# Kernel optimization log

Measured on AMD Instinct MI355X. Metric: run time of the kernel, lower is better.

The kernel has to match this reference:

```python
import jax, jax.numpy as jnp
import numpy as np

E = 1_000_000
C = 32
OUT = 64


def setup_inputs() -> dict:
    key = jax.random.key(0)
    k_x, k_nb, k_w, k_b = jax.random.split(key, 4)
    x = jax.random.normal(k_x, (E, C), dtype=jnp.float32)
    neighbors = jax.random.randint(k_nb, (E, 4), 0, E, dtype=jnp.int64)
    # Linear(5*C, OUT): weight [OUT, 5C], bias [OUT] (torch layout)
    bound = 1.0 / np.sqrt(5 * C)
    W = jax.random.uniform(k_w, (OUT, 5 * C), minval=-bound, maxval=bound, dtype=jnp.float32)
    b = jax.random.uniform(k_b, (OUT,), minval=-bound, maxval=bound, dtype=jnp.float32)
    return {"x": x, "neighbors": neighbors, "W": W, "b": b}


def reference(x, neighbors, W, b):
    # pad with a zero row so index -1 (clamped to 0 then masked) yields zeros
    padded = jnp.concatenate([x, jnp.zeros((1, x.shape[1]), dtype=x.dtype)], axis=0)
    safe = jnp.clip(neighbors, 0, None)
    nb = padded[safe]                                  # [E, 4, C]
    nb = jnp.where((neighbors < 0)[..., None], 0.0, nb)
    a0, a1, b0, b1 = nb[:, 0], nb[:, 1], nb[:, 2], nb[:, 3]
    desc_a = jnp.concatenate([a0 + a1, jnp.abs(a0 - a1)], axis=1)   # [E, 2C]
    desc_b = jnp.concatenate([b0 + b1, jnp.abs(b0 - b1)], axis=1)   # [E, 2C]
    combined = jnp.concatenate([x, desc_a + desc_b, jnp.abs(desc_a - desc_b)], axis=1)  # [E, 5C]
    return combined @ W.T + b
```

## Files before the change

kernel.cpp:

```cpp
#include <hip/hip_runtime.h>


typedef __bf16 bf16_t;
typedef __bf16 bf16x8 __attribute__((ext_vector_type(8)));
typedef float  f32x4  __attribute__((ext_vector_type(4)));

#define EC      1000000
#define CCH     32
#define OUTD    64
#define KD      160
#define MT      64
#define NTILES  (EC / MT)
#define NFRAG   1280

__global__ __launch_bounds__(256)
void meshconv_kernel(const float* __restrict__ x,
                     const int*   __restrict__ nbr,
                     const float* __restrict__ W,
                     const float* __restrict__ bias,
                     float*       __restrict__ out)
{
    __shared__ bf16_t w_lds[NFRAG * 8];

    const int tid  = threadIdx.x;
    const int wave = tid >> 6;
    const int lane = tid & 63;
    const int col  = lane & 15;
    const int quad = lane >> 4;

    for (int i = tid; i < NFRAG; i += 256) {
        const int fc  = i & 15;
        const int fq  = (i >> 4) & 3;
        const int ftn = (i >> 6) & 3;
        const int fks = i >> 8;
        const float* src = W + (ftn * 16 + fc) * KD + fks * 32 + fq * 8;
        f32x4 w0 = *(const f32x4*)src;
        f32x4 w1 = *(const f32x4*)(src + 4);
        bf16x8 wf;
        wf[0]=(bf16_t)w0[0]; wf[1]=(bf16_t)w0[1]; wf[2]=(bf16_t)w0[2]; wf[3]=(bf16_t)w0[3];
        wf[4]=(bf16_t)w1[0]; wf[5]=(bf16_t)w1[1]; wf[6]=(bf16_t)w1[2]; wf[7]=(bf16_t)w1[3];
        *(bf16x8*)&w_lds[i * 8] = wf;
    }

    float bv[4];
#pragma unroll
    for (int tn = 0; tn < 4; ++tn) bv[tn] = bias[tn * 16 + col];

    __syncthreads();

    for (int tile = blockIdx.x; tile < NTILES; tile += (int)gridDim.x) {
        const int e = tile * MT + wave * 16 + col;

        const int4 nb = ((const int4*)nbr)[e];
        const float m0 = nb.x < 0 ? 0.f : 1.f;
        const float m1 = nb.y < 0 ? 0.f : 1.f;
        const float m2 = nb.z < 0 ? 0.f : 1.f;
        const float m3 = nb.w < 0 ? 0.f : 1.f;
        const int i0 = nb.x < 0 ? 0 : nb.x;
        const int i1 = nb.y < 0 ? 0 : nb.y;
        const int i2 = nb.z < 0 ? 0 : nb.z;
        const int i3 = nb.w < 0 ? 0 : nb.w;

        const int co = quad * 8;
        const f32x4* px  = (const f32x4*)(x + (size_t)e  * CCH + co);
        const f32x4* pa0 = (const f32x4*)(x + (size_t)i0 * CCH + co);
        const f32x4* pa1 = (const f32x4*)(x + (size_t)i1 * CCH + co);
        const f32x4* pb0 = (const f32x4*)(x + (size_t)i2 * CCH + co);
        const f32x4* pb1 = (const f32x4*)(x + (size_t)i3 * CCH + co);

        f32x4 xv[2], a0[2], a1[2], b0[2], b1[2];
#pragma unroll
        for (int h = 0; h < 2; ++h) {
            xv[h] = px[h];
            a0[h] = pa0[h] * m0;
            a1[h] = pa1[h] * m1;
            b0[h] = pb0[h] * m2;
            b1[h] = pb1[h] * m3;
        }

        bf16x8 af[5];
#pragma unroll
        for (int h = 0; h < 2; ++h) {
#pragma unroll
            for (int j = 0; j < 4; ++j) {
                const int jj = h * 4 + j;
                const float sa = a0[h][j] + a1[h][j];
                const float da = fabsf(a0[h][j] - a1[h][j]);
                const float sb = b0[h][j] + b1[h][j];
                const float db = fabsf(b0[h][j] - b1[h][j]);
                af[0][jj] = (bf16_t)xv[h][j];
                af[1][jj] = (bf16_t)(sa + sb);
                af[2][jj] = (bf16_t)(da + db);
                af[3][jj] = (bf16_t)fabsf(sa - sb);
                af[4][jj] = (bf16_t)fabsf(da - db);
            }
        }

        f32x4 acc[4] = {{0.f,0.f,0.f,0.f},{0.f,0.f,0.f,0.f},
                        {0.f,0.f,0.f,0.f},{0.f,0.f,0.f,0.f}};
#pragma unroll
        for (int ks = 0; ks < 5; ++ks) {
#pragma unroll
            for (int tn = 0; tn < 4; ++tn) {
                const bf16x8 bfr = *(const bf16x8*)&w_lds[(((ks*4+tn)*4+quad)*16 + col) * 8];
                acc[tn] = __builtin_amdgcn_mfma_f32_16x16x32_bf16(af[ks], bfr, acc[tn], 0, 0, 0);
            }
        }

#pragma unroll
        for (int tn = 0; tn < 4; ++tn) {
            float* op = out + (size_t)(tile * MT + wave * 16 + quad * 4) * OUTD + tn * 16 + col;
#pragma unroll
            for (int r = 0; r < 4; ++r)
                __builtin_nontemporal_store(acc[tn][r] + bv[tn], op + (size_t)r * OUTD);
        }
    }
}

extern "C" void kernel_launch(void* const* d_in, const int* in_sizes, int n_in,
                              void* d_out, int out_size, void* d_ws, size_t ws_size,
                              hipStream_t stream) {
    const float* x    = (const float*)d_in[0];
    const int*   nbr  = (const int*)d_in[1];
    const float* W    = (const float*)d_in[2];
    const float* bias = (const float*)d_in[3];
    float* out = (float*)d_out;
    meshconv_kernel<<<dim3(3072), dim3(256), 0, stream>>>(x, nbr, W, bias, out);
}
```

Before: 436.6 us.

## Software-pipeline gathers across tiles and stage output through LDS for vector stores

Prefetches the next tile's neighbor indices and gathered rows into registers while the current tile is computed, so memory latency overlaps with the MFMA work. The accumulator results are transposed through a padded per-wave LDS buffer, which lets each lane write 16-byte contiguous nontemporal stores instead of scalar strided stores. The grid shrinks from 3072 to 1024 blocks so each block loops over more tiles. This raises register pressure from the doubled prefetch buffers, adds LDS traffic, and may reduce occupancy.

```diff
diff --git a/kernel.cpp b/kernel.cpp
--- a/kernel.cpp
+++ b/kernel.cpp
@@ -12,6 +12,8 @@
 #define MT      64
 #define NTILES  (EC / MT)
 #define NFRAG   1280
+#define TSTR    68
+#define GRID    1024
 
 __global__ __launch_bounds__(256)
 void meshconv_kernel(const float* __restrict__ x,
@@ -21,6 +23,7 @@
                      float*       __restrict__ out)
 {
     __shared__ bf16_t w_lds[NFRAG * 8];
+    __shared__ __attribute__((aligned(16))) float t_lds[4 * 16 * TSTR];
 
     const int tid  = threadIdx.x;
     const int wave = tid >> 6;
@@ -46,37 +49,41 @@
 #pragma unroll
     for (int tn = 0; tn < 4; ++tn) bv[tn] = bias[tn * 16 + col];
 
+    float* tw = &t_lds[wave * 16 * TSTR];
+
     __syncthreads();
 
-    for (int tile = blockIdx.x; tile < NTILES; tile += (int)gridDim.x) {
-        const int e = tile * MT + wave * 16 + col;
-
-        const int4 nb = ((const int4*)nbr)[e];
-        const float m0 = nb.x < 0 ? 0.f : 1.f;
-        const float m1 = nb.y < 0 ? 0.f : 1.f;
-        const float m2 = nb.z < 0 ? 0.f : 1.f;
-        const float m3 = nb.w < 0 ? 0.f : 1.f;
+    auto load_tile = [&](int t, int4& nb, f32x4* buf) {
+        const int e = t * MT + wave * 16 + col;
+        nb = ((const int4*)nbr)[e];
         const int i0 = nb.x < 0 ? 0 : nb.x;
         const int i1 = nb.y < 0 ? 0 : nb.y;
         const int i2 = nb.z < 0 ? 0 : nb.z;
         const int i3 = nb.w < 0 ? 0 : nb.w;
+        const int co = quad * 8;
+        const f32x4* p;
+        p = (const f32x4*)(x + (size_t)e  * CCH + co); buf[0] = p[0]; buf[1] = p[1];
+        p = (const f32x4*)(x + (size_t)i0 * CCH + co); buf[2] = p[0]; buf[3] = p[1];
+        p = (const f32x4*)(x + (size_t)i1 * CCH + co); buf[4] = p[0]; buf[5] = p[1];
+        p = (const f32x4*)(x + (size_t)i2 * CCH + co); buf[6] = p[0]; buf[7] = p[1];
+        p = (const f32x4*)(x + (size_t)i3 * CCH + co); buf[8] = p[0]; buf[9] = p[1];
+    };
 
-        const int co = quad * 8;
-        const f32x4* px  = (const f32x4*)(x + (size_t)e  * CCH + co);
-        const f32x4* pa0 = (const f32x4*)(x + (size_t)i0 * CCH + co);
-        const f32x4* pa1 = (const f32x4*)(x + (size_t)i1 * CCH + co);
-        const f32x4* pb0 = (const f32x4*)(x + (size_t)i2 * CCH + co);
-        const f32x4* pb1 = (const f32x4*)(x + (size_t)i3 * CCH + co);
+    int tile = blockIdx.x;
+    int4  nbc;
+    f32x4 cb[10];
+    if (tile < NTILES) load_tile(tile, nbc, cb);
 
-        f32x4 xv[2], a0[2], a1[2], b0[2], b1[2];
-#pragma unroll
-        for (int h = 0; h < 2; ++h) {
-            xv[h] = px[h];
-            a0[h] = pa0[h] * m0;
-            a1[h] = pa1[h] * m1;
-            b0[h] = pb0[h] * m2;
-            b1[h] = pb1[h] * m3;
-        }
+    for (; tile < NTILES; tile += GRID) {
+        const int nxt = tile + GRID;
+        int4  nbn;
+        f32x4 pb[10];
+        if (nxt < NTILES) load_tile(nxt, nbn, pb);
+
+        const float m0 = nbc.x < 0 ? 0.f : 1.f;
+        const float m1 = nbc.y < 0 ? 0.f : 1.f;
+        const float m2 = nbc.z < 0 ? 0.f : 1.f;
+        const float m3 = nbc.w < 0 ? 0.f : 1.f;
 
         bf16x8 af[5];
 #pragma unroll
@@ -84,11 +91,15 @@
 #pragma unroll
             for (int j = 0; j < 4; ++j) {
                 const int jj = h * 4 + j;
-                const float sa = a0[h][j] + a1[h][j];
-                const float da = fabsf(a0[h][j] - a1[h][j]);
-                const float sb = b0[h][j] + b1[h][j];
-                const float db = fabsf(b0[h][j] - b1[h][j]);
-                af[0][jj] = (bf16_t)xv[h][j];
+                const float va0 = cb[2 + h][j] * m0;
+                const float va1 = cb[4 + h][j] * m1;
+                const float vb0 = cb[6 + h][j] * m2;
+                const float vb1 = cb[8 + h][j] * m3;
+                const float sa = va0 + va1;
+                const float da = fabsf(va0 - va1);
+                const float sb = vb0 + vb1;
+                const float db = fabsf(vb0 - vb1);
+                af[0][jj] = (bf16_t)cb[h][j];
                 af[1][jj] = (bf16_t)(sa + sb);
                 af[2][jj] = (bf16_t)(da + db);
                 af[3][jj] = (bf16_t)fabsf(sa - sb);
@@ -108,12 +119,21 @@
         }
 
 #pragma unroll
-        for (int tn = 0; tn < 4; ++tn) {
-            float* op = out + (size_t)(tile * MT + wave * 16 + quad * 4) * OUTD + tn * 16 + col;
+        for (int tn = 0; tn < 4; ++tn)
 #pragma unroll
             for (int r = 0; r < 4; ++r)
-                __builtin_nontemporal_store(acc[tn][r] + bv[tn], op + (size_t)r * OUTD);
+                tw[(quad * 4 + r) * TSTR + tn * 16 + col] = acc[tn][r] + bv[tn];
+
+#pragma unroll
+        for (int r = 0; r < 4; ++r) {
+            const f32x4 v = *(const f32x4*)&tw[(quad * 4 + r) * TSTR + col * 4];
+            float* op = out + (size_t)(tile * MT + wave * 16 + quad * 4 + r) * OUTD + col * 4;
+            __builtin_nontemporal_store(v, (f32x4*)op);
         }
+
+        nbc = nbn;
+#pragma unroll
+        for (int k = 0; k < 10; ++k) cb[k] = pb[k];
     }
 }
 
@@ -125,5 +145,5 @@
     const float* W    = (const float*)d_in[2];
     const float* bias = (const float*)d_in[3];
     float* out = (float*)d_out;
-    meshconv_kernel<<<dim3(3072), dim3(256), 0, stream>>>(x, nbr, W, bias, out);
+    meshconv_kernel<<<dim3(GRID), dim3(256), 0, stream>>>(x, nbr, W, bias, out);
 }
```

Result: faster. 413.8 us (-5.2%).
